# Performance work log

Measured on AMD Instinct MI355X. Metric: run time of the kernel, lower is better.

The kernel has to match this reference:

```python
import jax, jax.numpy as jnp
import numpy as np
from jax import lax

ALPHA_LO = float(np.exp(-1.0 / 5.0))
ALPHA_HI = float(np.exp(-1.0 / 25.0))
THRESHOLD = 1.0


def setup_inputs() -> dict:
    key = jax.random.key(0)
    k1, k2, k3, k4, k5 = jax.random.split(key, 5)
    B, T, I, H = 64, 1024, 512, 512
    x = jax.random.normal(k1, (B, T, I), dtype=jnp.float32)
    # kaiming-uniform-like small init for Linear weight
    bound = 1.0 / np.sqrt(I)
    W = jax.random.uniform(k2, (H, I), minval=-bound, maxval=bound, dtype=jnp.float32)
    alpha = ALPHA_LO + jax.random.uniform(k3, (H,), dtype=jnp.float32) * (ALPHA_HI - ALPHA_LO)
    u0 = jax.random.uniform(k4, (B, H), dtype=jnp.float32)
    s0 = jax.random.uniform(k5, (B, H), dtype=jnp.float32)
    return {"x": x, "W": W, "alpha": alpha, "u0": u0, "s0": s0}


def reference(x, W, alpha, u0, s0):
    # x: [B, T, I], W: [H, I] (torch Linear layout), alpha/u0/s0 over H
    al = jnp.clip(alpha, ALPHA_LO, ALPHA_HI)  # [H]
    Wx = jnp.einsum('bti,hi->bth', x, W)      # [B, T, H]

    def step(carry, wx_t):
        u, s = carry
        u = al * (u - s) + (1.0 - al) * wx_t
        s = (u - THRESHOLD > 0).astype(wx_t.dtype)
        return (u, s), s

    _, spikes = lax.scan(step, (u0, s0), jnp.swapaxes(Wx, 0, 1))  # [T, B, H]
    return jnp.swapaxes(spikes, 0, 1)  # [B, T, H]
```

## Files before the change

kernel.cpp:

```cpp
#include <hip/hip_runtime.h>
#include <hip/hip_bf16.h>


#define ALPHA_LO_F ((float)0.8187307530779818)
#define ALPHA_HI_F ((float)0.9607894391523232)

typedef float v2f __attribute__((ext_vector_type(2)));

#define TM 128
#define TN 128
#define TK 16
__global__ __launch_bounds__(256) void gemm_nt_f32(
    const float* __restrict__ A,
    const float* __restrict__ B,
    float* __restrict__ C,
    int M, int N, int K)
{
    __shared__ float As[TK][TM];
    __shared__ float Bs[TK][TN];

    const int tid = threadIdx.x;
    const int m0  = blockIdx.y * TM;
    const int n0  = blockIdx.x * TN;

    const int lrow = tid >> 1;
    const int lkq  = (tid & 1) * 8;

    const int tm = tid >> 4;
    const int tn = tid & 15;

    v2f acc[8][4] = {};

    const float* Arow = A + (size_t)(m0 + lrow) * K + lkq;
    const float* Brow = B + (size_t)(n0 + lrow) * K + lkq;

    for (int k0 = 0; k0 < K; k0 += TK) {
        float4 av0 = *(const float4*)(Arow + k0);
        float4 av1 = *(const float4*)(Arow + k0 + 4);
        float4 bv0 = *(const float4*)(Brow + k0);
        float4 bv1 = *(const float4*)(Brow + k0 + 4);
        As[lkq + 0][lrow] = av0.x;  As[lkq + 1][lrow] = av0.y;
        As[lkq + 2][lrow] = av0.z;  As[lkq + 3][lrow] = av0.w;
        As[lkq + 4][lrow] = av1.x;  As[lkq + 5][lrow] = av1.y;
        As[lkq + 6][lrow] = av1.z;  As[lkq + 7][lrow] = av1.w;
        Bs[lkq + 0][lrow] = bv0.x;  Bs[lkq + 1][lrow] = bv0.y;
        Bs[lkq + 2][lrow] = bv0.z;  Bs[lkq + 3][lrow] = bv0.w;
        Bs[lkq + 4][lrow] = bv1.x;  Bs[lkq + 5][lrow] = bv1.y;
        Bs[lkq + 6][lrow] = bv1.z;  Bs[lkq + 7][lrow] = bv1.w;
        __syncthreads();

        #pragma unroll
        for (int k = 0; k < TK; ++k) {
            const float* Ak = &As[k][tm * 8];
            const float* Bk = &Bs[k][tn * 8];
            float4 a0 = *(const float4*)(Ak);
            float4 a1 = *(const float4*)(Ak + 4);
            float4 b0 = *(const float4*)(Bk);
            float4 b1 = *(const float4*)(Bk + 4);
            v2f bb[4];
            bb[0] = (v2f){b0.x, b0.y};  bb[1] = (v2f){b0.z, b0.w};
            bb[2] = (v2f){b1.x, b1.y};  bb[3] = (v2f){b1.z, b1.w};
            float a[8] = {a0.x, a0.y, a0.z, a0.w, a1.x, a1.y, a1.z, a1.w};
            #pragma unroll
            for (int i = 0; i < 8; ++i) {
                v2f ai = (v2f){a[i], a[i]};
                #pragma unroll
                for (int jv = 0; jv < 4; ++jv)
                    acc[i][jv] = __builtin_elementwise_fma(ai, bb[jv], acc[i][jv]);
            }
        }
        __syncthreads();
    }

    #pragma unroll
    for (int i = 0; i < 8; ++i) {
        float* Crow = C + (size_t)(m0 + tm * 8 + i) * N + n0 + tn * 8;
        float4 v0, v1;
        v0.x = acc[i][0].x; v0.y = acc[i][0].y; v0.z = acc[i][1].x; v0.w = acc[i][1].y;
        v1.x = acc[i][2].x; v1.y = acc[i][2].y; v1.z = acc[i][3].x; v1.w = acc[i][3].y;
        *(float4*)(Crow)     = v0;
        *(float4*)(Crow + 4) = v1;
    }
}

#define PF 32
__global__ __launch_bounds__(64) void lif_scan(
    float* __restrict__ buf,
    const float* __restrict__ alpha,
    const float* __restrict__ u0,
    const float* __restrict__ s0,
    int B, int T, int H)
{
    const int h = blockIdx.x * blockDim.x + threadIdx.x;
    const int b = blockIdx.y;
    if (h >= H) return;

    float al = alpha[h];
    al = fminf(fmaxf(al, ALPHA_LO_F), ALPHA_HI_F);
    const float one_m_al = 1.0f - al;

    float u = u0[(size_t)b * H + h];
    float s = s0[(size_t)b * H + h];

    const size_t sH = (size_t)H;
    size_t idx = (size_t)b * T * H + h;

    float cur[PF], nxt[PF];
    #pragma unroll
    for (int j = 0; j < PF; ++j) cur[j] = buf[idx + (size_t)j * sH];

    for (int t0 = 0; t0 < T; t0 += PF) {
        const size_t nidx = idx + (size_t)PF * sH;
        if (t0 + PF < T) {
            #pragma unroll
            for (int j = 0; j < PF; ++j) nxt[j] = buf[nidx + (size_t)j * sH];
        }
        #pragma unroll
        for (int j = 0; j < PF; ++j) {
            u = al * (u - s) + one_m_al * cur[j];
            s = (u - 1.0f > 0.0f) ? 1.0f : 0.0f;
            cur[j] = s;
        }
        #pragma unroll
        for (int j = 0; j < PF; ++j) buf[idx + (size_t)j * sH] = cur[j];
        #pragma unroll
        for (int j = 0; j < PF; ++j) cur[j] = nxt[j];
        idx = nidx;
    }
}

extern "C" void kernel_launch(void* const* d_in, const int* in_sizes, int n_in,
                              void* d_out, int out_size, void* d_ws, size_t ws_size,
                              hipStream_t stream) {
    const float* x     = (const float*)d_in[0];
    const float* W     = (const float*)d_in[1];
    const float* alpha = (const float*)d_in[2];
    const float* u0    = (const float*)d_in[3];
    const float* s0    = (const float*)d_in[4];
    float* out = (float*)d_out;

    const int H = in_sizes[2];
    const int I = in_sizes[1] / H;
    const int B = in_sizes[3] / H;
    const int T = in_sizes[0] / (B * I);
    const int M = B * T;

    dim3 grid1(H / TN, M / TM);
    gemm_nt_f32<<<grid1, 256, 0, stream>>>(x, W, out, M, H, I);

    dim3 grid2((H + 63) / 64, B);
    lif_scan<<<grid2, 64, 0, stream>>>(out, alpha, u0, s0, B, T, H);
}
```

Baseline: 617.6 us.

## Fuse GEMM and LIF scan into one kernel with per-chunk time tiles

```diff
diff --git a/kernel.cpp b/kernel.cpp
--- a/kernel.cpp
+++ b/kernel.cpp
@@ -2,130 +2,136 @@
 #include <hip/hip_bf16.h>
 
 
-#define ALPHA_LO_F ((float)0.8187307530779818)
-#define ALPHA_HI_F ((float)0.9607894391523232)
+#define ALPHA_LO_F 0.8187307530779818f
+#define ALPHA_HI_F 0.9607894391523232f
 
 typedef float v2f __attribute__((ext_vector_type(2)));
 
-#define TM 128
-#define TN 128
-#define TK 16
-__global__ __launch_bounds__(256) void gemm_nt_f32(
-    const float* __restrict__ A,
-    const float* __restrict__ B,
-    float* __restrict__ C,
-    int M, int N, int K)
+#define T_DIM 1024
+#define K_DIM 512
+#define H_DIM 512
+#define CT    256
+#define CH    128
+#define NCHK  (T_DIM / CT)
+#define BK    16
+#define APAD  260
+#define BPAD  132
+
+__global__ __launch_bounds__(512, 1) void lif_fused(
+    const float* __restrict__ x,
+    const float* __restrict__ W,
+    const float* __restrict__ alpha,
+    const float* __restrict__ u0,
+    const float* __restrict__ s0,
+    float* __restrict__ out)
 {
-    __shared__ float As[TK][TM];
-    __shared__ float Bs[TK][TN];
+    __shared__ float As[BK][APAD];
+    __shared__ float Bs[BK][BPAD];
+    __shared__ float u_s[CH], s_s[CH], al_s[CH];
 
     const int tid = threadIdx.x;
-    const int m0  = blockIdx.y * TM;
-    const int n0  = blockIdx.x * TN;
+    const int b   = blockIdx.x & 63;
+    const int hc  = blockIdx.x >> 6;
+    const int h0  = hc * CH;
 
-    const int lrow = tid >> 1;
-    const int lkq  = (tid & 1) * 8;
+    if (tid < CH) {
+        const int h = h0 + tid;
+        float a = alpha[h];
+        al_s[tid] = fminf(fmaxf(a, ALPHA_LO_F), ALPHA_HI_F);
+        u_s[tid] = u0[(size_t)b * H_DIM + h];
+        s_s[tid] = s0[(size_t)b * H_DIM + h];
+    }
 
     const int tm = tid >> 4;
     const int tn = tid & 15;
 
-    v2f acc[8][4] = {};
+    const float* xb = x + (size_t)b * T_DIM * K_DIM;
+    const float* Wc = W + (size_t)h0 * K_DIM;
 
-    const float* Arow = A + (size_t)(m0 + lrow) * K + lkq;
-    const float* Brow = B + (size_t)(n0 + lrow) * K + lkq;
+    __syncthreads();
 
-    for (int k0 = 0; k0 < K; k0 += TK) {
-        float4 av0 = *(const float4*)(Arow + k0);
-        float4 av1 = *(const float4*)(Arow + k0 + 4);
-        float4 bv0 = *(const float4*)(Brow + k0);
-        float4 bv1 = *(const float4*)(Brow + k0 + 4);
-        As[lkq + 0][lrow] = av0.x;  As[lkq + 1][lrow] = av0.y;
-        As[lkq + 2][lrow] = av0.z;  As[lkq + 3][lrow] = av0.w;
-        As[lkq + 4][lrow] = av1.x;  As[lkq + 5][lrow] = av1.y;
-        As[lkq + 6][lrow] = av1.z;  As[lkq + 7][lrow] = av1.w;
-        Bs[lkq + 0][lrow] = bv0.x;  Bs[lkq + 1][lrow] = bv0.y;
-        Bs[lkq + 2][lrow] = bv0.z;  Bs[lkq + 3][lrow] = bv0.w;
-        Bs[lkq + 4][lrow] = bv1.x;  Bs[lkq + 5][lrow] = bv1.y;
-        Bs[lkq + 6][lrow] = bv1.z;  Bs[lkq + 7][lrow] = bv1.w;
-        __syncthreads();
+    for (int c = 0; c < NCHK; ++c) {
+        const int t0 = c * CT;
 
-        #pragma unroll
-        for (int k = 0; k < TK; ++k) {
-            const float* Ak = &As[k][tm * 8];
-            const float* Bk = &Bs[k][tn * 8];
-            float4 a0 = *(const float4*)(Ak);
-            float4 a1 = *(const float4*)(Ak + 4);
-            float4 b0 = *(const float4*)(Bk);
-            float4 b1 = *(const float4*)(Bk + 4);
-            v2f bb[4];
-            bb[0] = (v2f){b0.x, b0.y};  bb[1] = (v2f){b0.z, b0.w};
-            bb[2] = (v2f){b1.x, b1.y};  bb[3] = (v2f){b1.z, b1.w};
-            float a[8] = {a0.x, a0.y, a0.z, a0.w, a1.x, a1.y, a1.z, a1.w};
+        v2f acc[8][4] = {};
+
+        for (int k0 = 0; k0 < K_DIM; k0 += BK) {
             #pragma unroll
-            for (int i = 0; i < 8; ++i) {
-                v2f ai = (v2f){a[i], a[i]};
+            for (int r = 0; r < 3; ++r) {
+                const int fid = tid + r * 512;
+                if (fid < 1024) {
+                    const int row = fid >> 2;
+                    const int kq  = (fid & 3) * 4;
+                    float4 v = *(const float4*)(xb + (size_t)(t0 + row) * K_DIM + k0 + kq);
+                    As[kq + 0][row] = v.x;  As[kq + 1][row] = v.y;
+                    As[kq + 2][row] = v.z;  As[kq + 3][row] = v.w;
+                } else {
+                    const int g   = fid - 1024;
+                    const int row = g >> 2;
+                    const int kq  = (g & 3) * 4;
+                    float4 v = *(const float4*)(Wc + (size_t)row * K_DIM + k0 + kq);
+                    Bs[kq + 0][row] = v.x;  Bs[kq + 1][row] = v.y;
+                    Bs[kq + 2][row] = v.z;  Bs[kq + 3][row] = v.w;
+                }
+            }
+            __syncthreads();
+
+            #pragma unroll
+            for (int k = 0; k < BK; ++k) {
+                const float* Ak = &As[k][tm * 8];
+                const float* Bk = &Bs[k][tn * 8];
+                float4 a0 = *(const float4*)(Ak);
+                float4 a1 = *(const float4*)(Ak + 4);
+                float4 b0 = *(const float4*)(Bk);
+                float4 b1 = *(const float4*)(Bk + 4);
+                v2f bb[4];
+                bb[0] = (v2f){b0.x, b0.y};  bb[1] = (v2f){b0.z, b0.w};
+                bb[2] = (v2f){b1.x, b1.y};  bb[3] = (v2f){b1.z, b1.w};
+                float a[8] = {a0.x, a0.y, a0.z, a0.w, a1.x, a1.y, a1.z, a1.w};
                 #pragma unroll
-                for (int jv = 0; jv < 4; ++jv)
-                    acc[i][jv] = __builtin_elementwise_fma(ai, bb[jv], acc[i][jv]);
+                for (int i = 0; i < 8; ++i) {
+                    v2f ai = (v2f){a[i], a[i]};
+                    #pragma unroll
+                    for (int jv = 0; jv < 4; ++jv)
+                        acc[i][jv] = __builtin_elementwise_fma(ai, bb[jv], acc[i][jv]);
+                }
             }
+            __syncthreads();
         }
-        __syncthreads();
-    }
 
-    #pragma unroll
-    for (int i = 0; i < 8; ++i) {
-        float* Crow = C + (size_t)(m0 + tm * 8 + i) * N + n0 + tn * 8;
-        float4 v0, v1;
-        v0.x = acc[i][0].x; v0.y = acc[i][0].y; v0.z = acc[i][1].x; v0.w = acc[i][1].y;
-        v1.x = acc[i][2].x; v1.y = acc[i][2].y; v1.z = acc[i][3].x; v1.w = acc[i][3].y;
-        *(float4*)(Crow)     = v0;
-        *(float4*)(Crow + 4) = v1;
-    }
-}
-
-#define PF 32
-__global__ __launch_bounds__(64) void lif_scan(
-    float* __restrict__ buf,
-    const float* __restrict__ alpha,
-    const float* __restrict__ u0,
-    const float* __restrict__ s0,
-    int B, int T, int H)
-{
-    const int h = blockIdx.x * blockDim.x + threadIdx.x;
-    const int b = blockIdx.y;
-    if (h >= H) return;
-
-    float al = alpha[h];
-    al = fminf(fmaxf(al, ALPHA_LO_F), ALPHA_HI_F);
-    const float one_m_al = 1.0f - al;
-
-    float u = u0[(size_t)b * H + h];
-    float s = s0[(size_t)b * H + h];
-
-    const size_t sH = (size_t)H;
-    size_t idx = (size_t)b * T * H + h;
-
-    float cur[PF], nxt[PF];
-    #pragma unroll
-    for (int j = 0; j < PF; ++j) cur[j] = buf[idx + (size_t)j * sH];
-
-    for (int t0 = 0; t0 < T; t0 += PF) {
-        const size_t nidx = idx + (size_t)PF * sH;
-        if (t0 + PF < T) {
-            #pragma unroll
-            for (int j = 0; j < PF; ++j) nxt[j] = buf[nidx + (size_t)j * sH];
+        for (int stage = 0; stage < 32; ++stage) {
+            if (tm == stage) {
+                const int hb = tn * 8;
+                float u[8], s[8], av[8], om[8];
+                #pragma unroll
+                for (int j = 0; j < 8; ++j) {
+                    u[j]  = u_s[hb + j];
+                    s[j]  = s_s[hb + j];
+                    av[j] = al_s[hb + j];
+                    om[j] = 1.0f - av[j];
+                }
+                #pragma unroll
+                for (int i = 0; i < 8; ++i) {
+                    float wx[8] = {acc[i][0].x, acc[i][0].y, acc[i][1].x, acc[i][1].y,
+                                   acc[i][2].x, acc[i][2].y, acc[i][3].x, acc[i][3].y};
+                    #pragma unroll
+                    for (int j = 0; j < 8; ++j) {
+                        u[j] = av[j] * (u[j] - s[j]) + om[j] * wx[j];
+                        s[j] = (u[j] - 1.0f > 0.0f) ? 1.0f : 0.0f;
+                    }
+                    const int t = t0 + stage * 8 + i;
+                    float* orow = out + ((size_t)b * T_DIM + t) * H_DIM + h0 + hb;
+                    *(float4*)(orow)     = make_float4(s[0], s[1], s[2], s[3]);
+                    *(float4*)(orow + 4) = make_float4(s[4], s[5], s[6], s[7]);
+                }
+                #pragma unroll
+                for (int j = 0; j < 8; ++j) {
+                    u_s[hb + j] = u[j];
+                    s_s[hb + j] = s[j];
+                }
+            }
+            __syncthreads();
         }
-        #pragma unroll
-        for (int j = 0; j < PF; ++j) {
-            u = al * (u - s) + one_m_al * cur[j];
-            s = (u - 1.0f > 0.0f) ? 1.0f : 0.0f;
-            cur[j] = s;
-        }
-        #pragma unroll
-        for (int j = 0; j < PF; ++j) buf[idx + (size_t)j * sH] = cur[j];
-        #pragma unroll
-        for (int j = 0; j < PF; ++j) cur[j] = nxt[j];
-        idx = nidx;
     }
 }
 
@@ -140,14 +146,8 @@
     float* out = (float*)d_out;
 
     const int H = in_sizes[2];
-    const int I = in_sizes[1] / H;
     const int B = in_sizes[3] / H;
-    const int T = in_sizes[0] / (B * I);
-    const int M = B * T;
+    const int grid = (H_DIM / CH) * B;
 
-    dim3 grid1(H / TN, M / TM);
-    gemm_nt_f32<<<grid1, 256, 0, stream>>>(x, W, out, M, H, I);
-
-    dim3 grid2((H + 63) / 64, B);
-    lif_scan<<<grid2, 64, 0, stream>>>(out, alpha, u0, s0, B, T, H);
+    lif_fused<<<grid, 512, 0, stream>>>(x, W, alpha, u0, s0, out);
 }
```

After: 726.0 us. 17.5% more time.
